# Kernel tuning notes

Hardware: AMD Instinct MI355X
Metric: run time of the kernel (lower is better)

Reference implementation:

```python
import jax, jax.numpy as jnp
import numpy as np

B, N, C = 16, 4096, 80
IOU_THR = 0.5
CONF_THR = 0.5
MAX_DET = 100
FROM_LOGITS = True


def setup_inputs() -> dict:
    key = jax.random.key(0)
    k1, k2 = jax.random.split(key)
    box_prediction = jax.random.uniform(k1, (B, N, 4), dtype=jnp.float32)
    class_prediction = jax.random.normal(k2, (B, N, C), dtype=jnp.float32)
    return {"box_prediction": box_prediction, "class_prediction": class_prediction}


def _pairwise_iou(b):
    # TF NMS kernel semantics: corners [y1,x1,y2,x2], normalized with min/max.
    y1 = jnp.minimum(b[:, 0], b[:, 2]); y2 = jnp.maximum(b[:, 0], b[:, 2])
    x1 = jnp.minimum(b[:, 1], b[:, 3]); x2 = jnp.maximum(b[:, 1], b[:, 3])
    area = (y2 - y1) * (x2 - x1)                      # [N]
    ih = jnp.maximum(0.0, jnp.minimum(y2[:, None], y2[None, :]) - jnp.maximum(y1[:, None], y1[None, :]))
    iw = jnp.maximum(0.0, jnp.minimum(x2[:, None], x2[None, :]) - jnp.maximum(x1[:, None], x1[None, :]))
    inter = ih * iw                                   # [N, N]
    union = area[:, None] + area[None, :] - inter
    return jnp.where(inter > 0.0, inter / union, 0.0)


def _nms_single(boxes, cls):
    # boxes [N,4], cls [N,C] -> padded ([MAX_DET,4], [MAX_DET,C])
    scores = jnp.max(cls, axis=1)                     # tf.reduce_max(cls_pred, axis=1)
    order = jnp.argsort(-scores)                      # descending, stable
    b = boxes[order]
    s = scores[order]
    valid = s > CONF_THR                              # score_threshold filter
    iou = _pairwise_iou(b)                            # [N, N]

    def body(keep, i):
        suppressed = jnp.any(keep & (iou[:, i] > IOU_THR))
        k = valid[i] & jnp.logical_not(suppressed)
        return keep.at[i].set(k), None

    keep, _ = jax.lax.scan(body, jnp.zeros(boxes.shape[0], dtype=bool), jnp.arange(boxes.shape[0]))
    # Compact kept boxes to the front (stable sort keeps descending-score order),
    # take the first MAX_DET slots, zero-pad the rest (fixed-shape analogue of
    # tf.image.non_max_suppression's variable-length index output).
    pos = jnp.argsort(jnp.logical_not(keep))[:MAX_DET]
    m = (jnp.arange(MAX_DET) < jnp.sum(keep))[:, None]
    out_idx = order[pos]
    nms_box = jnp.where(m, boxes[out_idx], 0.0)
    nms_cls = jnp.where(m, cls[out_idx], 0.0)
    return nms_box, nms_cls


def reference(box_prediction, class_prediction):
    # bounding_box_format == 'xywh' (absolute) -> convert_format is identity.
    if FROM_LOGITS:
        cls_predictions = jax.nn.softmax(jnp.square(class_prediction * 10.0), axis=-1)
    else:
        cls_predictions = class_prediction
    nms_box, nms_cls = jax.vmap(_nms_single)(box_prediction, cls_predictions)
    return nms_box, nms_cls, cls_predictions
```

## Files before the change

### kernel.cpp

```cpp
#include <hip/hip_runtime.h>
#include <cstdint>
#include <cstddef>

#define BB 16
#define NN 4096
#define CC 80
#define MAXD 100
#define CONF_T 0.5f
#define PER_B (MAXD * 4 + MAXD * CC)
#define NWORDS 64
#define FBCAP 2048
#define SEGSZ 2048
#define CH 1024
#define CCAP 1088

#define IOUC 0x1.000001p-1

#define WS_KEYS   0x000000
#define WS_NEED   0x200000

__global__ __launch_bounds__(256) void k_softmax(const float* __restrict__ cls_in,
                                                 float* __restrict__ probs,
                                                 uint64_t* __restrict__ keys) {
#pragma clang fp contract(off)
    int slot = blockIdx.x * 256 + threadIdx.x;
    int row  = slot >> 3;
    int j    = slot & 7;
    const float* rp = cls_in + (size_t)row * CC + j;

    float e[10];
    float m = -3.402823466e+38f;
    #pragma unroll
    for (int k = 0; k < 10; ++k) {
        float y = rp[8 * k] * 10.0f;
        float z = y * y;
        e[k] = z;
        m = fmaxf(m, z);
    }
    m = fmaxf(m, __shfl_xor(m, 1));
    m = fmaxf(m, __shfl_xor(m, 2));
    m = fmaxf(m, __shfl_xor(m, 4));

    #pragma unroll
    for (int k = 0; k < 10; ++k) e[k] = expf(e[k] - m);

    float acc = e[0];
    #pragma unroll
    for (int k = 1; k < 10; ++k) acc += e[k];
    acc = acc + __shfl_xor(acc, 1);
    acc = acc + __shfl_xor(acc, 2);
    acc = acc + __shfl_xor(acc, 4);

    float score = 1.0f / acc;
    float* pp = probs + (size_t)row * CC + j;
    #pragma unroll
    for (int k = 0; k < 10; ++k) pp[8 * k] = e[k] * score;

    if (j == 0) {
        unsigned n = (unsigned)(row & (NN - 1));
        keys[row] = ((uint64_t)__float_as_uint(score) << 32)
                  | (uint64_t)(0xFFFFFFFFu - n);
    }
}

__global__ __launch_bounds__(1024) void k_pnms(const uint64_t* __restrict__ keys,
                                               const float* __restrict__ boxes,
                                               const float* __restrict__ probs,
                                               float* __restrict__ out_box,
                                               float* __restrict__ out_cls) {
#pragma clang fp contract(off)
    __shared__ __align__(16) unsigned char sraw[6 * NN * 4];
    float* hy1 = (float*)sraw;
    float* hx1 = (float*)(sraw + NN * 4);
    float* hy2 = (float*)(sraw + 2 * NN * 4);
    float* hx2 = (float*)(sraw + 3 * NN * 4);
    float* har = (float*)(sraw + 4 * NN * 4);
    int*   og  = (int*)(sraw + 5 * NN * 4);
    uint64_t* bbuf = (uint64_t*)sraw;
    __shared__ int clist[CCAP];
    __shared__ uint64_t kill[64];
    __shared__ int cand_s[64];
    __shared__ int kpos[MAXD];
    __shared__ int wsumA[16], wsumB[16], wsumC[16];
    __shared__ int kept_s, fk0_s, done_s, ccnt_s, cur_s;

    const int tid = threadIdx.x, lane = tid & 63, wv = tid >> 6;
    const int b = blockIdx.x;
    const uint64_t* kb = keys + (size_t)b * NN;
    const float* bxp = boxes + (size_t)b * NN * 4;

    uint64_t myk[4]; bool fa[4], fb[4];
    int asum = 0, bsum = 0;
    for (int k = 0; k < 4; ++k) {
        uint64_t key = kb[4 * tid + k]; myk[k] = key;
        unsigned hi = (unsigned)(key >> 32);
        fa[k] = (hi == 0x3F800000u);
        fb[k] = (__uint_as_float(hi) > CONF_T) && !fa[k];
        asum += fa[k] ? 1 : 0; bsum += fb[k] ? 1 : 0;
    }
    int ia = asum, ib = bsum;
    for (int off = 1; off < 64; off <<= 1) {
        int va = __shfl_up(ia, off), vb = __shfl_up(ib, off);
        if (lane >= off) { ia += va; ib += vb; }
    }
    if (lane == 63) { wsumA[wv] = ia; wsumB[wv] = ib; }
    __syncthreads();
    int baseA = 0, baseB = 0, cntA = 0, cntB = 0;
    for (int w2 = 0; w2 < 16; ++w2) {
        if (w2 < wv) { baseA += wsumA[w2]; baseB += wsumB[w2]; }
        cntA += wsumA[w2]; cntB += wsumB[w2];
    }
    int pA = baseA + (ia - asum);
    int pB = baseB + (ib - bsum);
    for (int k = 0; k < 4; ++k) {
        if (fa[k]) og[pA++] = 4 * tid + k;
        if (fb[k]) bbuf[pB++] = myk[k];
    }
    __syncthreads();

    for (int i = tid; i < cntB; i += 1024) {
        uint64_t ki = bbuf[i];
        int rank = 0;
        for (int j = 0; j < cntB; ++j) rank += (bbuf[j] > ki) ? 1 : 0;
        og[cntA + rank] = (int)(0xFFFFFFFFu - (unsigned)(ki & 0xFFFFFFFFull));
    }
    int nl = cntA + cntB; if (nl > NN) nl = NN;
    __syncthreads();

    for (int i = tid; i < nl; i += 1024) {
        int o = og[i];
        float4 bv = ((const float4*)bxp)[o];
        float y1 = fminf(bv.x, bv.z), y2 = fmaxf(bv.x, bv.z);
        float x1 = fminf(bv.y, bv.w), x2 = fmaxf(bv.y, bv.w);
        hy1[i] = y1; hx1[i] = x1; hy2[i] = y2; hx2[i] = x2;
        har[i] = (y2 - y1) * (x2 - x1);
    }
    if (tid == 0) { kept_s = 0; fk0_s = 0; done_s = 0; ccnt_s = 0; cur_s = 0; }

    for (;;) {
        __syncthreads();
        for (;;) {
            int cc0 = ccnt_s, cur = cur_s;
            if (cc0 >= 64 || cur >= nl) break;
            int i = cur + tid;
            bool v = i < nl;
            int ii = v ? i : 0;
            float y1 = hy1[ii], x1 = hx1[ii], y2 = hy2[ii], x2 = hx2[ii], ar = har[ii];
            bool sup = false;
            int f1 = kept_s;
            for (int q0 = 0; q0 < f1; q0 += 64) {
                int qi = q0 + lane;
                int kp = (qi < f1) ? kpos[qi] : 0;
                float ky1 = hy1[kp], kx1 = hx1[kp], ky2 = hy2[kp], kx2 = hx2[kp], kar = har[kp];
                int qn = f1 - q0; if (qn > 64) qn = 64;
                bool deadall = false;
                for (int q = 0; q < qn; ++q) {
                    float qy1 = __shfl(ky1, q), qx1 = __shfl(kx1, q);
                    float qy2 = __shfl(ky2, q), qx2 = __shfl(kx2, q);
                    float qar = __shfl(kar, q);
                    float ih = fmaxf(0.f, fminf(y2, qy2) - fmaxf(y1, qy1));
                    float iw = fmaxf(0.f, fminf(x2, qx2) - fmaxf(x1, qx1));
                    float inter = ih * iw;
                    float uni = (ar + qar) - inter;
                    sup = sup || (inter > 0.f && (double)inter > (double)uni * IOUC);
                    if ((q & 7) == 7 && __ballot(v && !sup) == 0ull) { deadall = true; break; }
                }
                if (deadall) break;
            }
            bool srv = v && !sup;
            int sflag = srv ? 1 : 0;
            int inc = sflag;
            for (int off = 1; off < 64; off <<= 1) {
                int v2 = __shfl_up(inc, off);
                if (lane >= off) inc += v2;
            }
            if (lane == 63) wsumC[wv] = inc;
            __syncthreads();
            int base = 0, tot = 0;
            for (int w2 = 0; w2 < 16; ++w2) {
                int s2 = wsumC[w2];
                if (w2 < wv) base += s2;
                tot += s2;
            }
            if (srv) clist[cc0 + base + (inc - sflag)] = i;
            if (tid == 0) { ccnt_s = cc0 + tot; cur_s = cur + CH; }
            __syncthreads();
        }
        int cc = ccnt_s;
        int st = cc < 64 ? cc : 64;
        if (tid < 64) cand_s[tid] = (tid < st) ? clist[tid] : -1;
        __syncthreads();
        if (st <= 0) break;

        {
            int cj = cand_s[lane];
            bool jv = cj >= 0;
            int cjx = jv ? cj : 0;
            float jy1 = hy1[cjx], jx1 = hx1[cjx], jy2 = hy2[cjx], jx2 = hx2[cjx], jar = har[cjx];
            #pragma unroll
            for (int r = 0; r < 4; ++r) {
                int t = wv + 16 * r;
                int ct = cand_s[t];
                bool tv = ct >= 0;
                int ctx = tv ? ct : 0;
                float ty1 = hy1[ctx], tx1 = hx1[ctx], ty2 = hy2[ctx], tx2 = hx2[ctx], tar = har[ctx];
                float ih = fmaxf(0.f, fminf(ty2, jy2) - fmaxf(ty1, jy1));
                float iw = fmaxf(0.f, fminf(tx2, jx2) - fmaxf(tx1, jx1));
                float inter = ih * iw;
                float uni = (tar + jar) - inter;
                bool s = tv && jv && (inter > 0.f) && ((double)inter > (double)uni * IOUC);
                uint64_t w = __ballot(s);
                if (lane == 0) kill[t] = w;
            }
        }
        __syncthreads();
        if (wv == 0) {
            uint64_t suppressed = 0, keptmask = 0;
            for (int j2 = 0; j2 < st; ++j2) {
                if (!((suppressed >> j2) & 1ull)) {
                    keptmask |= 1ull << j2;
                    suppressed |= kill[j2];
                }
            }
            int k0 = kept_s;
            if ((keptmask >> lane) & 1ull) {
                int pos = k0 + __popcll(keptmask & ((1ull << lane) - 1ull));
                if (pos < MAXD) kpos[pos] = cand_s[lane];
            }
            int k1 = k0 + __popcll(keptmask);
            if (lane == 0) {
                fk0_s = k0;
                kept_s = k1;
                done_s = (k1 >= MAXD || cc < 64) ? 1 : 0;
            }
        }
        __syncthreads();
        if (done_s) break;

        {
            int f0 = fk0_s, f1 = kept_s;
            int j = st + tid;
            bool v = j < cc;
            int idx = v ? clist[j] : 0;
            float y1 = hy1[idx], x1 = hx1[idx], y2 = hy2[idx], x2 = hx2[idx], ar = har[idx];
            bool sup = false;
            for (int q0 = f0; q0 < f1; q0 += 64) {
                int qi = q0 + lane;
                int kp = (qi < f1) ? kpos[qi] : 0;
                float ky1 = hy1[kp], kx1 = hx1[kp], ky2 = hy2[kp], kx2 = hx2[kp], kar = har[kp];
                int qn = f1 - q0; if (qn > 64) qn = 64;
                bool deadall = false;
                for (int q = 0; q < qn; ++q) {
                    float qy1 = __shfl(ky1, q), qx1 = __shfl(kx1, q);
                    float qy2 = __shfl(ky2, q), qx2 = __shfl(kx2, q);
                    float qar = __shfl(kar, q);
                    float ih = fmaxf(0.f, fminf(y2, qy2) - fmaxf(y1, qy1));
                    float iw = fmaxf(0.f, fminf(x2, qx2) - fmaxf(x1, qx1));
                    float inter = ih * iw;
                    float uni = (ar + qar) - inter;
                    sup = sup || (inter > 0.f && (double)inter > (double)uni * IOUC);
                    if ((q & 7) == 7 && __ballot(v && !sup) == 0ull) { deadall = true; break; }
                }
                if (deadall) break;
            }
            bool srv = v && !sup;
            int sflag = srv ? 1 : 0;
            int inc = sflag;
            for (int off = 1; off < 64; off <<= 1) {
                int v2 = __shfl_up(inc, off);
                if (lane >= off) inc += v2;
            }
            if (lane == 63) wsumC[wv] = inc;
            __syncthreads();
            int base = 0, tot = 0;
            for (int w2 = 0; w2 < 16; ++w2) {
                int s2 = wsumC[w2];
                if (w2 < wv) base += s2;
                tot += s2;
            }
            if (srv) clist[base + (inc - sflag)] = idx;
            if (tid == 0) ccnt_s = tot;
        }
    }

    int kt = kept_s; if (kt > MAXD) kt = MAXD;
    if (tid < MAXD) clist[tid] = (tid < kt) ? og[kpos[tid]] : 0;
    __syncthreads();

    float* ob = out_box + (size_t)b * MAXD * 4;
    float* oc = out_cls + (size_t)b * MAXD * CC;
    const float* pb = probs + (size_t)b * NN * CC;
    for (int r = tid; r < MAXD * 4; r += 1024) {
        int t = r >> 2, e2 = r & 3;
        float val = 0.0f;
        if (t < kt) { int idx = clist[t]; val = bxp[(size_t)idx * 4 + e2]; }
        ob[r] = val;
    }
    for (int q = tid; q < MAXD * CC; q += 1024) {
        int t = q / CC, c = q - t * CC;
        float val = 0.0f;
        if (t < kt) { int idx = clist[t]; val = pb[(size_t)idx * CC + c]; }
        oc[q] = val;
    }
}

__global__ __launch_bounds__(256) void k_gather(const float* __restrict__ boxes,
                                                const float* __restrict__ probs,
                                                const int* __restrict__ kidx,
                                                const int* __restrict__ cnt,
                                                float* __restrict__ out_box,
                                                float* __restrict__ out_cls) {
    int u = blockIdx.x * 256 + threadIdx.x;
    if (u >= BB * PER_B) return;
    int b = u / PER_B;
    int r = u - b * PER_B;
    int count = cnt[b];
    float val = 0.0f;
    if (r < MAXD * 4) {
        int t = r >> 2, e = r & 3;
        if (t < count) {
            int idx = kidx[b * MAXD + t];
            val = boxes[((size_t)b * NN + idx) * 4 + e];
        }
        out_box[(size_t)b * MAXD * 4 + r] = val;
    } else {
        int q = r - MAXD * 4;
        int t = q / CC, c = q - t * CC;
        if (t < count) {
            int idx = kidx[b * MAXD + t];
            val = probs[((size_t)b * NN + idx) * CC + c];
        }
        out_cls[(size_t)b * MAXD * CC + q] = val;
    }
}

__global__ __launch_bounds__(1024) void k_nms_fb(uint64_t* keys,
                                                 const float* __restrict__ boxes,
                                                 int* __restrict__ kidx_out,
                                                 int* __restrict__ cnt_out) {
#pragma clang fp contract(off)
    __shared__ float sy1[SEGSZ], sx1[SEGSZ], sy2[SEGSZ], sx2[SEGSZ];
    __shared__ int   soidx[SEGSZ];
    __shared__ uint64_t bbuf[FBCAP];
    __shared__ uint64_t sup[NWORDS];
    __shared__ float ky1[MAXD], kx1[MAXD], ky2[MAXD], kx2[MAXD], kar[MAXD];
    __shared__ int   keptidx[MAXD];
    __shared__ int   wsumA[16], wsumB[16];
    __shared__ int   keptcnt_s, ctrl_s, seg_s;

    const int tid = threadIdx.x, lane = tid & 63, wv = tid >> 6;
    const int b = blockIdx.x;
    const uint64_t* kb = keys + (size_t)b * NN;
    const float* bxp = boxes + (size_t)b * NN * 4;
    int* og = (int*)(keys + (size_t)b * NN);

    uint64_t myk[4]; bool fa[4], fb[4];
    int asum = 0, bsum = 0;
    for (int k = 0; k < 4; ++k) {
        uint64_t key = kb[4 * tid + k]; myk[k] = key;
        unsigned hi = (unsigned)(key >> 32);
        fa[k] = (hi == 0x3F800000u);
        fb[k] = (__uint_as_float(hi) > CONF_T) && !fa[k];
        asum += fa[k] ? 1 : 0; bsum += fb[k] ? 1 : 0;
    }
    int ia = asum, ib = bsum;
    for (int off = 1; off < 64; off <<= 1) {
        int va = __shfl_up(ia, off), vb = __shfl_up(ib, off);
        if (lane >= off) { ia += va; ib += vb; }
    }
    if (lane == 63) { wsumA[wv] = ia; wsumB[wv] = ib; }
    __syncthreads();
    int baseA = 0, baseB = 0, cntA = 0, cntB = 0;
    for (int w2 = 0; w2 < 16; ++w2) {
        if (w2 < wv) { baseA += wsumA[w2]; baseB += wsumB[w2]; }
        cntA += wsumA[w2]; cntB += wsumB[w2];
    }
    int pA = baseA + (ia - asum);
    int pB = baseB + (ib - bsum);
    for (int k = 0; k < 4; ++k) {
        if (fa[k]) og[pA++] = 4 * tid + k;
        if (fb[k]) { if (pB < FBCAP) bbuf[pB] = myk[k]; pB++; }
    }
    int cntBc = cntB < FBCAP ? cntB : FBCAP;
    int nlist = cntA + cntBc;
    if (tid == 0) { keptcnt_s = 0; seg_s = 0; }
    for (int i = tid; i < FBCAP; i += 1024) if (i >= cntB) bbuf[i] = 0;
    __syncthreads();

    for (unsigned k2 = 2; k2 <= FBCAP; k2 <<= 1) {
        for (unsigned j = k2 >> 1; j > 0; j >>= 1) {
            for (unsigned i = tid; i < FBCAP; i += 1024) {
                unsigned p = i ^ j;
                if (p > i) {
                    uint64_t va = bbuf[i], vb = bbuf[p];
                    bool desc = ((i & k2) == 0);
                    if (desc ? (va < vb) : (va > vb)) { bbuf[i] = vb; bbuf[p] = va; }
                }
            }
            __syncthreads();
        }
    }
    for (int i = tid; i < cntBc; i += 1024)
        og[cntA + i] = (int)(0xFFFFFFFFu - (unsigned)(bbuf[i] & 0xFFFFFFFFull));
    if (tid < NWORDS) {
        int lo = tid * 64;
        uint64_t mm;
        if (nlist <= lo) mm = ~0ull;
        else if (nlist >= lo + 64) mm = 0ull;
        else mm = (~0ull) << (nlist - lo);
        sup[tid] = mm;
    }
    __syncthreads();

    for (int i = tid; i < SEGSZ; i += 1024) {
        if (i < nlist) {
            int o = og[i];
            soidx[i] = o;
            const float* bp = bxp + (size_t)o * 4;
            float b0 = bp[0], b1 = bp[1], b2 = bp[2], b3 = bp[3];
            sy1[i] = fminf(b0, b2); sy2[i] = fmaxf(b0, b2);
            sx1[i] = fminf(b1, b3); sx2[i] = fmaxf(b1, b3);
        }
    }
    __syncthreads();

    int curw = 0, segr = 0;
    while (true) {
        if (tid == 0) {
            int code = -1;
            for (;;) {
                int wend = (segr + 1) * (SEGSZ / 64);
                if (curw >= wend) {
                    if (segr == 0 && nlist > SEGSZ) {
                        code = -2; segr = 1; seg_s = 1; curw = SEGSZ / 64;
                    } else code = -1;
                    break;
                }
                uint64_t live = ~sup[curw];
                if (live) {
                    int j = __ffsll((unsigned long long)live) - 1;
                    int sel = curw * 64 + j;
                    int li = sel - segr * SEGSZ;
                    int kc = keptcnt_s;
                    keptidx[kc] = soidx[li];
                    ky1[kc] = sy1[li]; kx1[kc] = sx1[li];
                    ky2[kc] = sy2[li]; kx2[kc] = sx2[li];
                    kar[kc] = (sy2[li] - sy1[li]) * (sx2[li] - sx1[li]);
                    keptcnt_s = kc + 1;
                    sup[curw] |= (1ull << j);
                    code = (kc + 1 >= MAXD) ? -1 : sel;
                    break;
                }
                ++curw;
            }
            ctrl_s = code;
        }
        __syncthreads();
        int c = ctrl_s;
        if (c == -1) break;

        if (c == -2) {
            for (int i = tid; i < SEGSZ; i += 1024) {
                int gi = SEGSZ + i;
                if (gi < nlist) {
                    int o = og[gi];
                    soidx[i] = o;
                    const float* bp = bxp + (size_t)o * 4;
                    float b0 = bp[0], b1 = bp[1], b2 = bp[2], b3 = bp[3];
                    sy1[i] = fminf(b0, b2); sy2[i] = fmaxf(b0, b2);
                    sx1[i] = fminf(b1, b3); sx2[i] = fmaxf(b1, b3);
                }
            }
            __syncthreads();
            int kc = keptcnt_s;
            for (int k = 0; k < 2; ++k) {
                int li = tid + k * 1024;
                float y1 = sy1[li], y2 = sy2[li], x1 = sx1[li], x2 = sx2[li];
                float ar = (y2 - y1) * (x2 - x1);
                bool s = false;
                for (int q = 0; q < kc; ++q) {
                    float ih = fmaxf(0.f, fminf(y2, ky2[q]) - fmaxf(y1, ky1[q]));
                    float iw = fmaxf(0.f, fminf(x2, kx2[q]) - fmaxf(x1, kx1[q]));
                    float inter = ih * iw;
                    float uni = (ar + kar[q]) - inter;
                    s = s || (inter > 0.f && inter / uni > 0.5f);
                }
                uint64_t bal = __ballot(s);
                if (lane == 0 && bal) {
                    int word = (SEGSZ + k * 1024 + wv * 64) >> 6;
                    sup[word] |= bal;
                }
            }
            __syncthreads();
            continue;
        }

        int sg = seg_s;
        int cl = c - sg * SEGSZ;
        float cy1 = sy1[cl], cy2 = sy2[cl], cx1 = sx1[cl], cx2 = sx2[cl];
        float car = (cy2 - cy1) * (cx2 - cx1);
        for (int k = 0; k < 2; ++k) {
            int li = tid + k * 1024;
            float y1 = sy1[li], y2 = sy2[li], x1 = sx1[li], x2 = sx2[li];
            float ar = (y2 - y1) * (x2 - x1);
            float ih = fmaxf(0.f, fminf(y2, cy2) - fmaxf(y1, cy1));
            float iw = fmaxf(0.f, fminf(x2, cx2) - fmaxf(x1, cx1));
            float inter = ih * iw;
            float uni = (ar + car) - inter;
            bool s = (inter > 0.f) && (inter / uni > 0.5f);
            uint64_t bal = __ballot(s);
            if (lane == 0 && bal) {
                int word = (sg * SEGSZ + k * 1024 + wv * 64) >> 6;
                sup[word] |= bal;
            }
        }
        __syncthreads();
    }

    if (tid == 0) cnt_out[b] = keptcnt_s;
    for (int i = tid; i < MAXD; i += 1024)
        kidx_out[b * MAXD + i] = (i < keptcnt_s) ? keptidx[i] : 0;
}

extern "C" void kernel_launch(void* const* d_in, const int* in_sizes, int n_in,
                              void* d_out, int out_size, void* d_ws, size_t ws_size,
                              hipStream_t stream) {
    const float* boxes = (const float*)d_in[0];
    const float* cls   = (const float*)d_in[1];
    float* out = (float*)d_out;
    float* out_box = out;
    float* out_cls = out + (size_t)BB * MAXD * 4;
    float* probs   = out + (size_t)BB * MAXD * 4 + (size_t)BB * MAXD * CC;

    char* ws = (char*)d_ws;
    uint64_t* keys = (uint64_t*)(ws + WS_KEYS);

    k_softmax<<<(BB * NN * 8) / 256, 256, 0, stream>>>(cls, probs, keys);

    if (ws_size >= (size_t)WS_NEED) {
        k_pnms<<<BB, 1024, 0, stream>>>(keys, boxes, probs, out_box, out_cls);
    } else {
        int* kidx = (int*)(ws + (size_t)BB * NN * sizeof(uint64_t));
        int* cnt  = kidx + BB * MAXD;
        k_nms_fb<<<BB, 1024, 0, stream>>>(keys, boxes, kidx, cnt);
        k_gather<<<(BB * PER_B + 255) / 256, 256, 0, stream>>>(boxes, probs, kidx, cnt,
                                                               out_box, out_cls);
    }
}
```

Measured before the change: 116.4 us.

## Widen NMS candidate tile to 256 and cache kept boxes in shared arrays

Raises the per-round candidate tile from 64 to 256. The pairwise kill matrix becomes 256x256, built from boxes staged in shared memory, and the greedy resolve runs over four 64-bit words per row. Coordinates of kept boxes are copied into dedicated shared arrays, so suppression loops read them directly instead of gathering through kpos and shuffling. When nothing has been kept yet, the refill step skips the IoU test entirely. The aim is fewer serial rounds and barriers, at the cost of a longer single-wave resolve loop and more shared memory.

```diff
diff --git a/kernel.cpp b/kernel.cpp
--- a/kernel.cpp
+++ b/kernel.cpp
@@ -12,7 +12,8 @@
 #define FBCAP 2048
 #define SEGSZ 2048
 #define CH 1024
-#define CCAP 1088
+#define TK 256
+#define CCAP 1280
 
 #define IOUC 0x1.000001p-1
 
@@ -78,8 +79,10 @@
     int*   og  = (int*)(sraw + 5 * NN * 4);
     uint64_t* bbuf = (uint64_t*)sraw;
     __shared__ int clist[CCAP];
-    __shared__ uint64_t kill[64];
-    __shared__ int cand_s[64];
+    __shared__ uint64_t kill4[TK][4];
+    __shared__ int cand_s[TK];
+    __shared__ float scy1[TK], scx1[TK], scy2[TK], scx2[TK], scar[TK];
+    __shared__ float ky1[MAXD], kx1[MAXD], ky2[MAXD], kx2[MAXD], kar[MAXD];
     __shared__ int kpos[MAXD];
     __shared__ int wsumA[16], wsumB[16], wsumC[16];
     __shared__ int kept_s, fk0_s, done_s, ccnt_s, cur_s;
@@ -141,31 +144,31 @@
         __syncthreads();
         for (;;) {
             int cc0 = ccnt_s, cur = cur_s;
-            if (cc0 >= 64 || cur >= nl) break;
+            if (cc0 >= TK || cur >= nl) break;
             int i = cur + tid;
             bool v = i < nl;
+            int f1 = kept_s;
+            if (f1 == 0) {
+                if (v) clist[cc0 + tid] = i;
+                if (tid == 0) {
+                    int rem = nl - cur;
+                    ccnt_s = cc0 + (rem < CH ? rem : CH);
+                    cur_s = cur + CH;
+                }
+                __syncthreads();
+                continue;
+            }
             int ii = v ? i : 0;
             float y1 = hy1[ii], x1 = hx1[ii], y2 = hy2[ii], x2 = hx2[ii], ar = har[ii];
             bool sup = false;
-            int f1 = kept_s;
-            for (int q0 = 0; q0 < f1; q0 += 64) {
-                int qi = q0 + lane;
-                int kp = (qi < f1) ? kpos[qi] : 0;
-                float ky1 = hy1[kp], kx1 = hx1[kp], ky2 = hy2[kp], kx2 = hx2[kp], kar = har[kp];
-                int qn = f1 - q0; if (qn > 64) qn = 64;
-                bool deadall = false;
-                for (int q = 0; q < qn; ++q) {
-                    float qy1 = __shfl(ky1, q), qx1 = __shfl(kx1, q);
-                    float qy2 = __shfl(ky2, q), qx2 = __shfl(kx2, q);
-                    float qar = __shfl(kar, q);
-                    float ih = fmaxf(0.f, fminf(y2, qy2) - fmaxf(y1, qy1));
-                    float iw = fmaxf(0.f, fminf(x2, qx2) - fmaxf(x1, qx1));
-                    float inter = ih * iw;
-                    float uni = (ar + qar) - inter;
-                    sup = sup || (inter > 0.f && (double)inter > (double)uni * IOUC);
-                    if ((q & 7) == 7 && __ballot(v && !sup) == 0ull) { deadall = true; break; }
-                }
-                if (deadall) break;
+            for (int q = 0; q < f1; ++q) {
+                float qy1 = ky1[q], qx1 = kx1[q], qy2 = ky2[q], qx2 = kx2[q], qar = kar[q];
+                float ih = fmaxf(0.f, fminf(y2, qy2) - fmaxf(y1, qy1));
+                float iw = fmaxf(0.f, fminf(x2, qx2) - fmaxf(x1, qx1));
+                float inter = ih * iw;
+                float uni = (ar + qar) - inter;
+                sup = sup || (inter > 0.f && (double)inter > (double)uni * IOUC);
+                if ((q & 15) == 15 && __ballot(v && !sup) == 0ull) break;
             }
             bool srv = v && !sup;
             int sflag = srv ? 1 : 0;
@@ -187,51 +190,135 @@
             __syncthreads();
         }
         int cc = ccnt_s;
-        int st = cc < 64 ? cc : 64;
-        if (tid < 64) cand_s[tid] = (tid < st) ? clist[tid] : -1;
+        int st = cc < TK ? cc : TK;
+        if (tid < TK) {
+            int c = (tid < st) ? clist[tid] : -1;
+            cand_s[tid] = c;
+            int cx = c >= 0 ? c : 0;
+            scy1[tid] = hy1[cx]; scx1[tid] = hx1[cx];
+            scy2[tid] = hy2[cx]; scx2[tid] = hx2[cx];
+            scar[tid] = har[cx];
+        }
         __syncthreads();
         if (st <= 0) break;
 
         {
-            int cj = cand_s[lane];
-            bool jv = cj >= 0;
-            int cjx = jv ? cj : 0;
-            float jy1 = hy1[cjx], jx1 = hx1[cjx], jy2 = hy2[cjx], jx2 = hx2[cjx], jar = har[cjx];
+            float jy1[4], jx1[4], jy2[4], jx2[4], jar[4]; bool jv[4];
             #pragma unroll
-            for (int r = 0; r < 4; ++r) {
-                int t = wv + 16 * r;
-                int ct = cand_s[t];
-                bool tv = ct >= 0;
-                int ctx = tv ? ct : 0;
-                float ty1 = hy1[ctx], tx1 = hx1[ctx], ty2 = hy2[ctx], tx2 = hx2[ctx], tar = har[ctx];
-                float ih = fmaxf(0.f, fminf(ty2, jy2) - fmaxf(ty1, jy1));
-                float iw = fmaxf(0.f, fminf(tx2, jx2) - fmaxf(tx1, jx1));
-                float inter = ih * iw;
-                float uni = (tar + jar) - inter;
-                bool s = tv && jv && (inter > 0.f) && ((double)inter > (double)uni * IOUC);
-                uint64_t w = __ballot(s);
-                if (lane == 0) kill[t] = w;
+            for (int w = 0; w < 4; ++w) {
+                int j = 64 * w + lane;
+                jv[w] = cand_s[j] >= 0;
+                jy1[w] = scy1[j]; jx1[w] = scx1[j];
+                jy2[w] = scy2[j]; jx2[w] = scx2[j]; jar[w] = scar[j];
+            }
+            #pragma unroll
+            for (int r = 0; r < 16; ++r) {
+                int t = wv * 16 + r;
+                bool tv = cand_s[t] >= 0;
+                float ty1 = scy1[t], tx1 = scx1[t], ty2 = scy2[t], tx2 = scx2[t], tar = scar[t];
+                #pragma unroll
+                for (int w = 0; w < 4; ++w) {
+                    float ih = fmaxf(0.f, fminf(ty2, jy2[w]) - fmaxf(ty1, jy1[w]));
+                    float iw = fmaxf(0.f, fminf(tx2, jx2[w]) - fmaxf(tx1, jx1[w]));
+                    float inter = ih * iw;
+                    float uni = (tar + jar[w]) - inter;
+                    bool s = tv && jv[w] && (inter > 0.f) && ((double)inter > (double)uni * IOUC);
+                    uint64_t bal = __ballot(s);
+                    if (lane == 0) kill4[t][w] = bal;
+                }
             }
         }
         __syncthreads();
         if (wv == 0) {
-            uint64_t suppressed = 0, keptmask = 0;
-            for (int j2 = 0; j2 < st; ++j2) {
-                if (!((suppressed >> j2) & 1ull)) {
-                    keptmask |= 1ull << j2;
-                    suppressed |= kill[j2];
+            uint64_t s0 = 0, s1 = 0, s2 = 0, s3 = 0;
+            uint64_t m0 = 0, m1 = 0, m2 = 0, m3 = 0;
+            {
+                int lim = st < 64 ? st : 64;
+                for (int jj = 0; jj < lim; ++jj) {
+                    uint64_t kk0 = kill4[jj][0], kk1 = kill4[jj][1];
+                    uint64_t kk2 = kill4[jj][2], kk3 = kill4[jj][3];
+                    if (!((s0 >> jj) & 1ull)) {
+                        m0 |= 1ull << jj; s0 |= kk0; s1 |= kk1; s2 |= kk2; s3 |= kk3;
+                    }
+                }
+            }
+            if (st > 64) {
+                int lim = st - 64; if (lim > 64) lim = 64;
+                for (int jj = 0; jj < lim; ++jj) {
+                    int j = 64 + jj;
+                    uint64_t kk0 = kill4[j][0], kk1 = kill4[j][1];
+                    uint64_t kk2 = kill4[j][2], kk3 = kill4[j][3];
+                    if (!((s1 >> jj) & 1ull)) {
+                        m1 |= 1ull << jj; s0 |= kk0; s1 |= kk1; s2 |= kk2; s3 |= kk3;
+                    }
+                }
+            }
+            if (st > 128) {
+                int lim = st - 128; if (lim > 64) lim = 64;
+                for (int jj = 0; jj < lim; ++jj) {
+                    int j = 128 + jj;
+                    uint64_t kk0 = kill4[j][0], kk1 = kill4[j][1];
+                    uint64_t kk2 = kill4[j][2], kk3 = kill4[j][3];
+                    if (!((s2 >> jj) & 1ull)) {
+                        m2 |= 1ull << jj; s0 |= kk0; s1 |= kk1; s2 |= kk2; s3 |= kk3;
+                    }
+                }
+            }
+            if (st > 192) {
+                int lim = st - 192; if (lim > 64) lim = 64;
+                for (int jj = 0; jj < lim; ++jj) {
+                    int j = 192 + jj;
+                    uint64_t kk0 = kill4[j][0], kk1 = kill4[j][1];
+                    uint64_t kk2 = kill4[j][2], kk3 = kill4[j][3];
+                    if (!((s3 >> jj) & 1ull)) {
+                        m3 |= 1ull << jj; s0 |= kk0; s1 |= kk1; s2 |= kk2; s3 |= kk3;
+                    }
                 }
             }
             int k0 = kept_s;
-            if ((keptmask >> lane) & 1ull) {
-                int pos = k0 + __popcll(keptmask & ((1ull << lane) - 1ull));
-                if (pos < MAXD) kpos[pos] = cand_s[lane];
-            }
-            int k1 = k0 + __popcll(keptmask);
+            int c0 = __popcll(m0), c1 = __popcll(m1), c2 = __popcll(m2), c3 = __popcll(m3);
+            uint64_t below = (1ull << lane) - 1ull;
+            if ((m0 >> lane) & 1ull) {
+                int pos = k0 + __popcll(m0 & below);
+                if (pos < MAXD) {
+                    int j = lane;
+                    kpos[pos] = cand_s[j];
+                    ky1[pos] = scy1[j]; kx1[pos] = scx1[j];
+                    ky2[pos] = scy2[j]; kx2[pos] = scx2[j]; kar[pos] = scar[j];
+                }
+            }
+            if ((m1 >> lane) & 1ull) {
+                int pos = k0 + c0 + __popcll(m1 & below);
+                if (pos < MAXD) {
+                    int j = 64 + lane;
+                    kpos[pos] = cand_s[j];
+                    ky1[pos] = scy1[j]; kx1[pos] = scx1[j];
+                    ky2[pos] = scy2[j]; kx2[pos] = scx2[j]; kar[pos] = scar[j];
+                }
+            }
+            if ((m2 >> lane) & 1ull) {
+                int pos = k0 + c0 + c1 + __popcll(m2 & below);
+                if (pos < MAXD) {
+                    int j = 128 + lane;
+                    kpos[pos] = cand_s[j];
+                    ky1[pos] = scy1[j]; kx1[pos] = scx1[j];
+                    ky2[pos] = scy2[j]; kx2[pos] = scx2[j]; kar[pos] = scar[j];
+                }
+            }
+            if ((m3 >> lane) & 1ull) {
+                int pos = k0 + c0 + c1 + c2 + __popcll(m3 & below);
+                if (pos < MAXD) {
+                    int j = 192 + lane;
+                    kpos[pos] = cand_s[j];
+                    ky1[pos] = scy1[j]; kx1[pos] = scx1[j];
+                    ky2[pos] = scy2[j]; kx2[pos] = scx2[j]; kar[pos] = scar[j];
+                }
+            }
             if (lane == 0) {
+                int k1 = k0 + c0 + c1 + c2 + c3;
                 fk0_s = k0;
                 kept_s = k1;
-                done_s = (k1 >= MAXD || cc < 64) ? 1 : 0;
+                done_s = (k1 >= MAXD || cc < TK) ? 1 : 0;
             }
         }
         __syncthreads();
@@ -244,24 +331,14 @@
             int idx = v ? clist[j] : 0;
             float y1 = hy1[idx], x1 = hx1[idx], y2 = hy2[idx], x2 = hx2[idx], ar = har[idx];
             bool sup = false;
-            for (int q0 = f0; q0 < f1; q0 += 64) {
-                int qi = q0 + lane;
-                int kp = (qi < f1) ? kpos[qi] : 0;
-                float ky1 = hy1[kp], kx1 = hx1[kp], ky2 = hy2[kp], kx2 = hx2[kp], kar = har[kp];
-                int qn = f1 - q0; if (qn > 64) qn = 64;
-                bool deadall = false;
-                for (int q = 0; q < qn; ++q) {
-                    float qy1 = __shfl(ky1, q), qx1 = __shfl(kx1, q);
-                    float qy2 = __shfl(ky2, q), qx2 = __shfl(kx2, q);
-                    float qar = __shfl(kar, q);
-                    float ih = fmaxf(0.f, fminf(y2, qy2) - fmaxf(y1, qy1));
-                    float iw = fmaxf(0.f, fminf(x2, qx2) - fmaxf(x1, qx1));
-                    float inter = ih * iw;
-                    float uni = (ar + qar) - inter;
-                    sup = sup || (inter > 0.f && (double)inter > (double)uni * IOUC);
-                    if ((q & 7) == 7 && __ballot(v && !sup) == 0ull) { deadall = true; break; }
-                }
-                if (deadall) break;
+            for (int q = f0; q < f1; ++q) {
+                float qy1 = ky1[q], qx1 = kx1[q], qy2 = ky2[q], qx2 = kx2[q], qar = kar[q];
+                float ih = fmaxf(0.f, fminf(y2, qy2) - fmaxf(y1, qy1));
+                float iw = fmaxf(0.f, fminf(x2, qx2) - fmaxf(x1, qx1));
+                float inter = ih * iw;
+                float uni = (ar + qar) - inter;
+                sup = sup || (inter > 0.f && (double)inter > (double)uni * IOUC);
+                if (((q - f0) & 15) == 15 && __ballot(v && !sup) == 0ull) break;
             }
             bool srv = v && !sup;
             int sflag = srv ? 1 : 0;
```

Result: no change. 116.7 us (+0.2%).

## Replace chunked candidate-list NMS with per-64-box group sweep against kept set

Applied to the files above, without the earlier changes.

Rewrites the greedy NMS loop in k_pnms. The old version compacted survivors over 1024-wide chunks into a candidate list, then resolved them 64 at a time. The new version walks the score-sorted boxes in groups of 64. For each group, all 16 waves test it in parallel against the kept boxes, which are now cached as compact coordinate arrays in shared memory, and a single wave then resolves suppression inside the group with a 64x64 kill-mask scan. This removes the prefix-sum compaction passes and the indirect kpos gathers, at the cost of one or two block barriers per 64 boxes and possibly many groups when most boxes get suppressed.

```diff
diff --git a/kernel.cpp b/kernel.cpp
--- a/kernel.cpp
+++ b/kernel.cpp
@@ -11,8 +11,6 @@
 #define NWORDS 64
 #define FBCAP 2048
 #define SEGSZ 2048
-#define CH 1024
-#define CCAP 1088
 
 #define IOUC 0x1.000001p-1
 
@@ -77,12 +75,13 @@
     float* har = (float*)(sraw + 4 * NN * 4);
     int*   og  = (int*)(sraw + 5 * NN * 4);
     uint64_t* bbuf = (uint64_t*)sraw;
-    __shared__ int clist[CCAP];
     __shared__ uint64_t kill[64];
-    __shared__ int cand_s[64];
+    __shared__ uint64_t persup[16];
+    __shared__ float ky1[MAXD], kx1[MAXD], ky2[MAXD], kx2[MAXD], kar[MAXD];
     __shared__ int kpos[MAXD];
-    __shared__ int wsumA[16], wsumB[16], wsumC[16];
-    __shared__ int kept_s, fk0_s, done_s, ccnt_s, cur_s;
+    __shared__ int fidx[MAXD];
+    __shared__ int wsumA[16], wsumB[16];
+    __shared__ int kept_s, done_s;
 
     const int tid = threadIdx.x, lane = tid & 63, wv = tid >> 6;
     const int b = blockIdx.x;
@@ -135,156 +134,85 @@
         hy1[i] = y1; hx1[i] = x1; hy2[i] = y2; hx2[i] = x2;
         har[i] = (y2 - y1) * (x2 - x1);
     }
-    if (tid == 0) { kept_s = 0; fk0_s = 0; done_s = 0; ccnt_s = 0; cur_s = 0; }
-
-    for (;;) {
-        __syncthreads();
-        for (;;) {
-            int cc0 = ccnt_s, cur = cur_s;
-            if (cc0 >= 64 || cur >= nl) break;
-            int i = cur + tid;
-            bool v = i < nl;
-            int ii = v ? i : 0;
-            float y1 = hy1[ii], x1 = hx1[ii], y2 = hy2[ii], x2 = hx2[ii], ar = har[ii];
-            bool sup = false;
-            int f1 = kept_s;
-            for (int q0 = 0; q0 < f1; q0 += 64) {
-                int qi = q0 + lane;
-                int kp = (qi < f1) ? kpos[qi] : 0;
-                float ky1 = hy1[kp], kx1 = hx1[kp], ky2 = hy2[kp], kx2 = hx2[kp], kar = har[kp];
-                int qn = f1 - q0; if (qn > 64) qn = 64;
-                bool deadall = false;
-                for (int q = 0; q < qn; ++q) {
-                    float qy1 = __shfl(ky1, q), qx1 = __shfl(kx1, q);
-                    float qy2 = __shfl(ky2, q), qx2 = __shfl(kx2, q);
-                    float qar = __shfl(kar, q);
-                    float ih = fmaxf(0.f, fminf(y2, qy2) - fmaxf(y1, qy1));
-                    float iw = fmaxf(0.f, fminf(x2, qx2) - fmaxf(x1, qx1));
-                    float inter = ih * iw;
-                    float uni = (ar + qar) - inter;
-                    sup = sup || (inter > 0.f && (double)inter > (double)uni * IOUC);
-                    if ((q & 7) == 7 && __ballot(v && !sup) == 0ull) { deadall = true; break; }
-                }
-                if (deadall) break;
-            }
-            bool srv = v && !sup;
-            int sflag = srv ? 1 : 0;
-            int inc = sflag;
-            for (int off = 1; off < 64; off <<= 1) {
-                int v2 = __shfl_up(inc, off);
-                if (lane >= off) inc += v2;
-            }
-            if (lane == 63) wsumC[wv] = inc;
-            __syncthreads();
-            int base = 0, tot = 0;
-            for (int w2 = 0; w2 < 16; ++w2) {
-                int s2 = wsumC[w2];
-                if (w2 < wv) base += s2;
-                tot += s2;
-            }
-            if (srv) clist[cc0 + base + (inc - sflag)] = i;
-            if (tid == 0) { ccnt_s = cc0 + tot; cur_s = cur + CH; }
-            __syncthreads();
-        }
-        int cc = ccnt_s;
-        int st = cc < 64 ? cc : 64;
-        if (tid < 64) cand_s[tid] = (tid < st) ? clist[tid] : -1;
-        __syncthreads();
-        if (st <= 0) break;
-
-        {
-            int cj = cand_s[lane];
-            bool jv = cj >= 0;
-            int cjx = jv ? cj : 0;
-            float jy1 = hy1[cjx], jx1 = hx1[cjx], jy2 = hy2[cjx], jx2 = hx2[cjx], jar = har[cjx];
-            #pragma unroll
-            for (int r = 0; r < 4; ++r) {
-                int t = wv + 16 * r;
-                int ct = cand_s[t];
-                bool tv = ct >= 0;
-                int ctx = tv ? ct : 0;
-                float ty1 = hy1[ctx], tx1 = hx1[ctx], ty2 = hy2[ctx], tx2 = hx2[ctx], tar = har[ctx];
-                float ih = fmaxf(0.f, fminf(ty2, jy2) - fmaxf(ty1, jy1));
-                float iw = fmaxf(0.f, fminf(tx2, jx2) - fmaxf(tx1, jx1));
-                float inter = ih * iw;
-                float uni = (tar + jar) - inter;
-                bool s = tv && jv && (inter > 0.f) && ((double)inter > (double)uni * IOUC);
-                uint64_t w = __ballot(s);
-                if (lane == 0) kill[t] = w;
-            }
-        }
-        __syncthreads();
-        if (wv == 0) {
-            uint64_t suppressed = 0, keptmask = 0;
-            for (int j2 = 0; j2 < st; ++j2) {
-                if (!((suppressed >> j2) & 1ull)) {
-                    keptmask |= 1ull << j2;
-                    suppressed |= kill[j2];
-                }
-            }
-            int k0 = kept_s;
-            if ((keptmask >> lane) & 1ull) {
-                int pos = k0 + __popcll(keptmask & ((1ull << lane) - 1ull));
-                if (pos < MAXD) kpos[pos] = cand_s[lane];
-            }
-            int k1 = k0 + __popcll(keptmask);
-            if (lane == 0) {
-                fk0_s = k0;
-                kept_s = k1;
-                done_s = (k1 >= MAXD || cc < 64) ? 1 : 0;
-            }
-        }
+    if (tid == 0) { kept_s = 0; done_s = 0; }
+
+    int ng = (nl + 63) >> 6;
+    for (int g = 0; g < ng; ++g) {
         __syncthreads();
         if (done_s) break;
-
-        {
-            int f0 = fk0_s, f1 = kept_s;
-            int j = st + tid;
-            bool v = j < cc;
-            int idx = v ? clist[j] : 0;
-            float y1 = hy1[idx], x1 = hx1[idx], y2 = hy2[idx], x2 = hx2[idx], ar = har[idx];
-            bool sup = false;
-            for (int q0 = f0; q0 < f1; q0 += 64) {
-                int qi = q0 + lane;
-                int kp = (qi < f1) ? kpos[qi] : 0;
-                float ky1 = hy1[kp], kx1 = hx1[kp], ky2 = hy2[kp], kx2 = hx2[kp], kar = har[kp];
-                int qn = f1 - q0; if (qn > 64) qn = 64;
-                bool deadall = false;
-                for (int q = 0; q < qn; ++q) {
-                    float qy1 = __shfl(ky1, q), qx1 = __shfl(kx1, q);
-                    float qy2 = __shfl(ky2, q), qx2 = __shfl(kx2, q);
-                    float qar = __shfl(kar, q);
-                    float ih = fmaxf(0.f, fminf(y2, qy2) - fmaxf(y1, qy1));
-                    float iw = fmaxf(0.f, fminf(x2, qx2) - fmaxf(x1, qx1));
-                    float inter = ih * iw;
-                    float uni = (ar + qar) - inter;
-                    sup = sup || (inter > 0.f && (double)inter > (double)uni * IOUC);
-                    if ((q & 7) == 7 && __ballot(v && !sup) == 0ull) { deadall = true; break; }
-                }
-                if (deadall) break;
-            }
-            bool srv = v && !sup;
-            int sflag = srv ? 1 : 0;
-            int inc = sflag;
-            for (int off = 1; off < 64; off <<= 1) {
-                int v2 = __shfl_up(inc, off);
-                if (lane >= off) inc += v2;
-            }
-            if (lane == 63) wsumC[wv] = inc;
-            __syncthreads();
-            int base = 0, tot = 0;
-            for (int w2 = 0; w2 < 16; ++w2) {
-                int s2 = wsumC[w2];
-                if (w2 < wv) base += s2;
-                tot += s2;
-            }
-            if (srv) clist[base + (inc - sflag)] = idx;
-            if (tid == 0) ccnt_s = tot;
-        }
-    }
+        int kt = kept_s;
+        int i = g * 64 + lane;
+        bool v = i < nl;
+        int ii = v ? i : 0;
+        float y1 = hy1[ii], x1 = hx1[ii], y2 = hy2[ii], x2 = hx2[ii], ar = har[ii];
+
+        bool killed = false;
+        for (int q = wv; q < kt; q += 16) {
+            float qy1 = ky1[q], qx1 = kx1[q], qy2 = ky2[q], qx2 = kx2[q], qar = kar[q];
+            float ih = fmaxf(0.f, fminf(y2, qy2) - fmaxf(y1, qy1));
+            float iw = fmaxf(0.f, fminf(x2, qx2) - fmaxf(x1, qx1));
+            float inter = ih * iw;
+            float uni = (ar + qar) - inter;
+            killed = killed || (inter > 0.f && (double)inter > (double)uni * IOUC);
+        }
+        uint64_t pw = __ballot((!v) || killed);
+        if (lane == 0) persup[wv] = pw;
+        __syncthreads();
+        uint64_t sup0 = 0;
+        #pragma unroll
+        for (int w2 = 0; w2 < 16; ++w2) sup0 |= persup[w2];
+        if (sup0 == ~0ull) continue;
+
+        #pragma unroll
+        for (int r = 0; r < 4; ++r) {
+            int t = wv + 16 * r;
+            int it = g * 64 + t;
+            bool tv = it < nl;
+            int itx = tv ? it : 0;
+            float ty1 = hy1[itx], tx1 = hx1[itx], ty2 = hy2[itx], tx2 = hx2[itx], tar = har[itx];
+            float ih = fmaxf(0.f, fminf(ty2, y2) - fmaxf(ty1, y1));
+            float iw = fmaxf(0.f, fminf(tx2, x2) - fmaxf(tx1, x1));
+            float inter = ih * iw;
+            float uni = (tar + ar) - inter;
+            bool s = tv && v && (inter > 0.f) && ((double)inter > (double)uni * IOUC);
+            uint64_t w = __ballot(s);
+            if (lane == 0) kill[t] = w;
+        }
+        __syncthreads();
+
+        if (wv == 0) {
+            uint64_t sup = sup0, keptm = 0;
+            #pragma unroll
+            for (int c8 = 0; c8 < 8; ++c8) {
+                uint64_t kk[8];
+                #pragma unroll
+                for (int u = 0; u < 8; ++u) kk[u] = kill[c8 * 8 + u];
+                #pragma unroll
+                for (int u = 0; u < 8; ++u) {
+                    int t = c8 * 8 + u;
+                    if (!((sup >> t) & 1ull)) { keptm |= 1ull << t; sup |= kk[u]; }
+                }
+            }
+            int k0 = kept_s;
+            if ((keptm >> lane) & 1ull) {
+                int pos = k0 + __popcll(keptm & ((1ull << lane) - 1ull));
+                if (pos < MAXD) {
+                    kpos[pos] = i;
+                    ky1[pos] = y1; kx1[pos] = x1;
+                    ky2[pos] = y2; kx2[pos] = x2; kar[pos] = ar;
+                }
+            }
+            if (lane == 0) {
+                int k1 = k0 + __popcll(keptm);
+                kept_s = k1;
+                done_s = (k1 >= MAXD) ? 1 : 0;
+            }
+        }
+    }
+    __syncthreads();
 
     int kt = kept_s; if (kt > MAXD) kt = MAXD;
-    if (tid < MAXD) clist[tid] = (tid < kt) ? og[kpos[tid]] : 0;
+    if (tid < MAXD) fidx[tid] = (tid < kt) ? og[kpos[tid]] : 0;
     __syncthreads();
 
     float* ob = out_box + (size_t)b * MAXD * 4;
@@ -293,13 +221,13 @@
     for (int r = tid; r < MAXD * 4; r += 1024) {
         int t = r >> 2, e2 = r & 3;
         float val = 0.0f;
-        if (t < kt) { int idx = clist[t]; val = bxp[(size_t)idx * 4 + e2]; }
+        if (t < kt) { int idx = fidx[t]; val = bxp[(size_t)idx * 4 + e2]; }
         ob[r] = val;
     }
     for (int q = tid; q < MAXD * CC; q += 1024) {
         int t = q / CC, c = q - t * CC;
         float val = 0.0f;
-        if (t < kt) { int idx = clist[t]; val = pb[(size_t)idx * CC + c]; }
+        if (t < kt) { int idx = fidx[t]; val = pb[(size_t)idx * CC + c]; }
         oc[q] = val;
     }
 }
```

Result: faster. 100.9 us (-13.3%).
